# Optimization experiments

Hardware: AMD Instinct MI355X
Metric: run time of the kernel (lower is better)

Reference implementation:

```python
import jax, jax.numpy as jnp
import numpy as np

N = 2048
E_HALF = 65536
THRESHOLD = 0.8


def _segment_softmax(e, seg, n):
    e = e - jax.ops.segment_max(e, seg, num_segments=n)[seg]
    w = jnp.exp(e)
    return w / (jax.ops.segment_sum(w, seg, num_segments=n)[seg] + 1e-16)


def _forward(edge_index, x, mask, Wg1, bg1, Wg2, bg2, Wa1, asrc1, adst1, ba1,
             Wa2, asrc2, adst2, ba2, Wq, bq, Wk, bk, Wv, bv, Wo, bo,
             Wtq, btq, Wtk, btk, Wtv, btv, Wts, bts, W1, b1, W2, b2, Wc, bc):
    n = x.shape[0]
    src, dst = edge_index[0], edge_index[1]

    # dense adjacency (edge_index is symmetric by construction)
    A = jnp.zeros((n, n), jnp.float32).at[src, dst].add(1.0)
    deg = A.sum(axis=1)
    dinv = jnp.where(deg > 0, jax.lax.rsqrt(jnp.maximum(deg, 1e-12)), 0.0)
    # sym-normalized Laplacian L = I - D^-1/2 A D^-1/2 (get_laplacian + to_dense_adj)
    L = jnp.eye(n, dtype=jnp.float32) - dinv[:, None] * A * dinv[None, :]
    _, evecs = jnp.linalg.eigh(L)
    lap_ev = jax.lax.stop_gradient(evecs[:, :2])  # k=2 eigenvectors; data-only, no grad
    x_combined = jnp.concatenate([x, lap_ev], axis=1)  # [n, 5]

    # GCN uncertainty net (torch.no_grad in source)
    A2 = A + jnp.eye(n, dtype=jnp.float32)
    d2 = jax.lax.rsqrt(A2.sum(axis=1))
    Ahat = d2[:, None] * A2 * d2[None, :]

    def gcn(h):
        z = jax.nn.relu(Ahat @ (h @ Wg1) + bg1)
        return (Ahat @ (z @ Wg2) + bg2)[:, 0]

    # add_self_loops
    sl = jnp.arange(n)
    s2 = jnp.concatenate([src, sl])
    d2e = jnp.concatenate([dst, sl])

    def gat(h, W, a_s, a_d, b):
        hw = h @ W                                   # [n, F]
        al = hw @ a_s
        ad = hw @ a_d
        e = jax.nn.leaky_relu(al[s2] + ad[d2e], 0.2)  # per-edge score
        a = _segment_softmax(e, d2e, n)               # softmax over incoming edges
        return jax.ops.segment_sum(a[:, None] * hw[s2], d2e, num_segments=n) + b

    h = jax.nn.relu(gat(x_combined, Wa1, asrc1, adst1, ba1))  # GAT layer 1
    h = gat(h, Wa2, asrc2, adst2, ba2)                        # GAT layer 2 -> [n, 5]

    # nn.MultiheadAttention over all n nodes (seq=n, batch=1, 1 head, d=5)
    q = h @ Wq + bq
    k = h @ Wk + bk
    v = h @ Wv + bv
    attn = jax.nn.softmax((q @ k.T) / np.float32(np.sqrt(5.0)), axis=-1)  # [n, n]
    h = (attn @ v) @ Wo + bo

    # TransformerConv(5, 5, heads=1) with root_weight skip
    tq = h @ Wtq + btq
    tk = h @ Wtk + btk
    tv = h @ Wtv + btv
    e = (tq[d2e] * tk[s2]).sum(-1) / np.float32(np.sqrt(5.0))
    a = _segment_softmax(e, d2e, n)
    xt = jax.ops.segment_sum(a[:, None] * tv[s2], d2e, num_segments=n) + (h @ Wts + bts)

    # MLPAggregation with index=arange(n): each node alone at slot 0 of its group,
    # so flatten([n, n, 5]) @ W1 reduces exactly to xt @ W1[:5]
    hm = jax.nn.relu(xt @ W1[:5] + b1)
    logits = hm @ W2 + b2                            # [n, n]

    # get_safe_logits (torch.no_grad block)
    u = jax.lax.stop_gradient(gcn(xt))               # [n]
    h_t = THRESHOLD - u.max()
    crit = jnp.argmax(u)
    logits = logits.at[crit].add(jnp.where(h_t < 0.2, jnp.float32(10.0), jnp.float32(0.0)))

    masked_logits = logits * mask[None, :]           # broadcast over last dim (torch semantics)
    value = (logits @ Wc + bc).mean()
    return masked_logits, value, x_combined


def setup_inputs() -> dict:
    key = jax.random.key(0)
    ks = jax.random.split(key, 24)

    def w(k, shape, fan_in):
        return jax.random.normal(k, shape, jnp.float32) / np.float32(np.sqrt(fan_in))

    x = jax.random.uniform(ks[0], (N, 3), dtype=jnp.float32)
    e = jax.random.randint(ks[1], (2, E_HALF), 0, N)
    edge_index = jnp.concatenate([e, e[::-1]], axis=1)  # symmetrized -> [2, 2*E_HALF]
    mask = (jax.random.uniform(ks[2], (N,)) > 0.5).astype(jnp.float32)
    return dict(
        x=x, edge_index=edge_index, mask=mask,
        Wg1=w(ks[3], (5, 16), 5), bg1=jnp.zeros(16), Wg2=w(ks[4], (16, 1), 16), bg2=jnp.zeros(1),
        Wa1=w(ks[5], (5, 8), 5), asrc1=w(ks[6], (8,), 8), adst1=w(ks[7], (8,), 8), ba1=jnp.zeros(8),
        Wa2=w(ks[8], (8, 5), 8), asrc2=w(ks[9], (5,), 5), adst2=w(ks[10], (5,), 5), ba2=jnp.zeros(5),
        Wq=w(ks[11], (5, 5), 5), bq=jnp.zeros(5), Wk=w(ks[12], (5, 5), 5), bk=jnp.zeros(5),
        Wv=w(ks[13], (5, 5), 5), bv=jnp.zeros(5), Wo=w(ks[14], (5, 5), 5), bo=jnp.zeros(5),
        Wtq=w(ks[15], (5, 5), 5), btq=jnp.zeros(5), Wtk=w(ks[16], (5, 5), 5), btk=jnp.zeros(5),
        Wtv=w(ks[17], (5, 5), 5), btv=jnp.zeros(5), Wts=w(ks[18], (5, 5), 5), bts=jnp.zeros(5),
        W1=w(ks[19], (5 * N, 64), 5 * N), b1=jnp.zeros(64),
        W2=w(ks[20], (64, N), 64), b2=jnp.zeros(N),
        Wc=w(ks[21], (N, 1), N), bc=jnp.zeros(1))


def reference(x, edge_index, mask, Wg1, bg1, Wg2, bg2, Wa1, asrc1, adst1, ba1,
              Wa2, asrc2, adst2, ba2, Wq, bq, Wk, bk, Wv, bv, Wo, bo,
              Wtq, btq, Wtk, btk, Wtv, btv, Wts, bts, W1, b1, W2, b2, Wc, bc):
    return _forward(edge_index, x, mask, Wg1, bg1, Wg2, bg2, Wa1, asrc1, adst1, ba1,
                    Wa2, asrc2, adst2, ba2, Wq, bq, Wk, bk, Wv, bv, Wo, bo,
                    Wtq, btq, Wtk, btk, Wtv, btv, Wts, bts, W1, b1, W2, b2, Wc, bc)
```

## Files before the change

kernel.cpp:

```cpp
#include <hip/hip_runtime.h>
#include <math.h>


#define N    2048
#define NE   131072
#define KL   64
#define TPB  256
#define NB   16
#define CH   (N/NB)

#define SIGN1 -1.0f
#define SIGN2 -1.0f

__device__ __forceinline__ unsigned fkey(float f){
  unsigned u = __float_as_uint(f);
  return (u & 0x80000000u) ? ~u : (u | 0x80000000u);
}
__device__ __forceinline__ float fkeyinv(unsigned k){
  unsigned u = (k & 0x80000000u) ? (k ^ 0x80000000u) : ~k;
  return __uint_as_float(u);
}
__device__ __forceinline__ unsigned wang(unsigned s){
  s = (s ^ 61u) ^ (s >> 16); s *= 9u; s ^= s >> 4; s *= 0x27d4eb2du; s ^= s >> 15;
  return s;
}
__device__ __forceinline__ float block_sum(float v, float* sh){
  __syncthreads();
  for (int off = 32; off > 0; off >>= 1) v += __shfl_down(v, off);
  int lane = threadIdx.x & 63, w = threadIdx.x >> 6;
  if (lane == 0) sh[w] = v;
  __syncthreads();
  return sh[0] + sh[1] + sh[2] + sh[3];
}

__device__ __forceinline__ float aloadf(const float* p){
  return __hip_atomic_load(p, __ATOMIC_RELAXED, __HIP_MEMORY_SCOPE_AGENT);
}
__device__ __forceinline__ void astoref(float* p, float v){
  __hip_atomic_store(p, v, __ATOMIC_RELAXED, __HIP_MEMORY_SCOPE_AGENT);
}
__device__ __forceinline__ unsigned aloadu(const unsigned* p){
  return __hip_atomic_load(p, __ATOMIC_RELAXED, __HIP_MEMORY_SCOPE_AGENT);
}
__device__ __forceinline__ int aloadi(const int* p){
  return __hip_atomic_load(p, __ATOMIC_RELAXED, __HIP_MEMORY_SCOPE_AGENT);
}
__device__ __forceinline__ void astorei(int* p, int v){
  __hip_atomic_store(p, v, __ATOMIC_RELAXED, __HIP_MEMORY_SCOPE_AGENT);
}
__device__ __forceinline__ float2 aload2(const float* p){
  unsigned long long v = __hip_atomic_load((const unsigned long long*)p,
                         __ATOMIC_RELAXED, __HIP_MEMORY_SCOPE_AGENT);
  return make_float2(__uint_as_float((unsigned)v),
                     __uint_as_float((unsigned)(v >> 32)));
}
__device__ __forceinline__ void astore2(float* p, float a, float b){
  unsigned long long v = ((unsigned long long)__float_as_uint(b) << 32)
                       | (unsigned long long)__float_as_uint(a);
  __hip_atomic_store((unsigned long long*)p, v,
                     __ATOMIC_RELAXED, __HIP_MEMORY_SCOPE_AGENT);
}

__device__ __forceinline__ void gbar(unsigned* cnt, unsigned* gen, unsigned* phase){
  __syncthreads();
  if (threadIdx.x == 0){
    unsigned p = ++(*phase);
    __atomic_signal_fence(__ATOMIC_SEQ_CST);
    __builtin_amdgcn_s_waitcnt(0);
    unsigned old = __hip_atomic_fetch_add(cnt, 1u, __ATOMIC_RELAXED, __HIP_MEMORY_SCOPE_AGENT);
    if (old == p*NB - 1u){
      __hip_atomic_store(gen, p, __ATOMIC_RELAXED, __HIP_MEMORY_SCOPE_AGENT);
    } else {
      while (__hip_atomic_load(gen, __ATOMIC_RELAXED, __HIP_MEMORY_SCOPE_AGENT) < p)
        __builtin_amdgcn_s_sleep(1);
    }
    __atomic_signal_fence(__ATOMIC_SEQ_CST);
  }
  __syncthreads();
}

__global__ void k_init(float* deg, float* scal, unsigned* bar){
  int i = blockIdx.x*TPB + threadIdx.x;
  if (i < N) deg[i] = 0.f;
  if (i < 16) scal[i] = 0.f;
  if (i < 64) bar[i] = 0u;
}
__global__ void k_deg(const int* ei, float* deg){
  int e = blockIdx.x*TPB + threadIdx.x;
  if (e < NE) atomicAdd(&deg[ei[e]], 1.0f);
}
__global__ void k_nodeinit(const float* deg, float* dinv, float* d2g, float* v1){
  int i = blockIdx.x*TPB + threadIdx.x;
  if (i < N){
    float d = deg[i];
    dinv[i] = d > 0.f ? rsqrtf(d) : 0.f;
    d2g[i]  = rsqrtf(d + 1.f);
    v1[i]   = sqrtf(d / (float)NE);
  }
}
__global__ void k_rowptr(const float* deg, int* rowptr, int* fill){
  __shared__ int part[256];
  __shared__ int off[257];
  int t = threadIdx.x;
  int base = t*8;
  int local[8];
  int s = 0;
  for (int k = 0; k < 8; k++){ local[k] = s; s += (int)deg[base + k]; }
  part[t] = s;
  __syncthreads();
  if (t == 0){ off[0] = 0; for (int i = 0; i < 256; i++) off[i+1] = off[i] + part[i]; }
  __syncthreads();
  int o = off[t];
  for (int k = 0; k < 8; k++){ int v = o + local[k]; rowptr[base+k] = v; fill[base+k] = v; }
  if (t == 255) rowptr[N] = off[256];
}
__global__ void k_csr(const int* ei, int* fill, int* cols){
  int e = blockIdx.x*TPB + threadIdx.x;
  if (e < NE){
    int s = ei[e];
    int pos = atomicAdd(&fill[s], 1);
    cols[pos] = ei[NE + e];
  }
}

__global__ __launch_bounds__(256) void k_lanczos(
    const int* __restrict__ rowptr, const int* __restrict__ cols,
    const float* __restrict__ dinv, const float* __restrict__ v1,
    const float* __restrict__ x,
    float* Qsl, float* yG, float* parts, float* parts2, float* npart,
    float* alpha, float* beta, float* zsm, float* v2, float* xc,
    float* outbuf, float* scal, unsigned* mkv, int* v2i, unsigned* bar){
  __shared__ __align__(16) float ybuf[N];
  __shared__ __align__(16) float yl[CH];
  __shared__ float cb[KL+2], cb2[KL+2];
  __shared__ float npl[NB];
  __shared__ float zl[KL];
  __shared__ float sh[4];
  __shared__ unsigned mkl;
  __shared__ double ta[KL], tb2[KL];
  unsigned* cnt = bar;
  unsigned* gen = bar + 32;
  unsigned phase = 0;
  const int tid = threadIdx.x, blk = blockIdx.x;
  const int base = blk*CH;
  float* Qb = Qsl + (size_t)blk*KL*CH;
  float* ssq = scal + 3;

  if (tid < CH){
    float r = (float)(wang(base + tid) & 0xffffffu) * (2.f/16777216.f) - 1.f;
    yl[tid] = r;
  }
  __syncthreads();
  {
    float p = (tid < CH) ? v1[base + tid]*yl[tid] : 0.f;
    float s = block_sum(p, sh);
    if (tid == 0) astoref(&parts[blk], s);
  }
  gbar(cnt, gen, &phase);
  {
    if (tid < NB) npl[tid] = aloadf(&parts[tid]);
    __syncthreads();
    float c = 0.f;
    for (int b = 0; b < NB; b++) c += npl[b];
    float acc = 0.f;
    if (tid < CH){
      float v = yl[tid] - c*v1[base + tid];
      yl[tid] = v;
      acc = v*v;
    }
    __syncthreads();
    if (tid < CH/2) astore2(yG + base + 2*tid, yl[2*tid], yl[2*tid+1]);
    float s = block_sum(acc, sh);
    if (tid == 0) astoref(&npart[blk], s);
  }
  gbar(cnt, gen, &phase);

  for (int j = 0; j < KL; j++){
    {
      for (int t = tid; t < N/2; t += TPB){
        float2 v = aload2(yG + 2*t);
        ybuf[2*t] = v.x; ybuf[2*t+1] = v.y;
      }
      if (tid < NB/2){
        float2 v = aload2(npart + 2*tid);
        npl[2*tid] = v.x; npl[2*tid+1] = v.y;
      }
    }
    __syncthreads();
    {
      float ss = 0.f;
      for (int b = 0; b < NB; b++) ss += npl[b];
      float rn = rsqrtf(ss);
      if (blk == 0 && tid == 0 && j > 0) beta[j-1] = sqrtf(ss);
      int r = tid >> 1;
      int half = tid & 1;
      int row = base + r;
      int b0 = rowptr[row], b1 = rowptr[row+1];
      float sg = 0.f;
      for (int p = b0 + half; p < b1; p += 2){
        int c = cols[p];
        sg += dinv[c]*ybuf[c];
      }
      sg += __shfl_down(sg, 1);
      if (half == 0){
        float q = rn*ybuf[row];
        Qb[(size_t)j*CH + r] = q;
        yl[r] = q - dinv[row]*rn*sg;
      }
    }
    __syncthreads();
    if (tid <= j+1){
      float d = 0.f;
      const float4* y4 = (const float4*)yl;
      if (tid <= j){
        const float4* q4 = (const float4*)(Qb + (size_t)tid*CH);
        for (int e = 0; e < CH/4; e++){
          float4 q = q4[e], yv = y4[e];
          d += q.x*yv.x + q.y*yv.y + q.z*yv.z + q.w*yv.w;
        }
      } else {
        const float4* v4 = (const float4*)(v1 + base);
        for (int e = 0; e < CH/4; e++){
          float4 q = v4[e], yv = y4[e];
          d += q.x*yv.x + q.y*yv.y + q.z*yv.z + q.w*yv.w;
        }
      }
      astoref(&parts[tid*NB + blk], d);
    }
    gbar(cnt, gen, &phase);
    if (tid <= j+1){
      const float* pr = parts + tid*NB;
      float s = 0.f;
      for (int b = 0; b < NB/2; b++){
        float2 v = aload2(pr + 2*b);
        s += v.x + v.y;
      }
      cb[tid] = s;
    }
    __syncthreads();
    {
      int e = tid >> 1, h = tid & 1;
      float a2 = 0.f;
      for (int i = h; i <= j+1; i += 2)
        a2 += cb[i] * ((i <= j) ? Qb[(size_t)i*CH + e] : v1[base + e]);
      a2 += __shfl_down(a2, 1);
      if (h == 0) yl[e] -= a2;
    }
    __syncthreads();
    if (tid <= j+1){
      float d = 0.f;
      const float4* y4 = (const float4*)yl;
      if (tid <= j){
        const float4* q4 = (const float4*)(Qb + (size_t)tid*CH);
        for (int e = 0; e < CH/4; e++){
          float4 q = q4[e], yv = y4[e];
          d += q.x*yv.x + q.y*yv.y + q.z*yv.z + q.w*yv.w;
        }
      } else {
        const float4* v4 = (const float4*)(v1 + base);
        for (int e = 0; e < CH/4; e++){
          float4 q = v4[e], yv = y4[e];
          d += q.x*yv.x + q.y*yv.y + q.z*yv.z + q.w*yv.w;
        }
      }
      astoref(&parts2[tid*NB + blk], d);
    }
    gbar(cnt, gen, &phase);
    if (tid <= j+1){
      const float* pr = parts2 + tid*NB;
      float s = 0.f;
      for (int b = 0; b < NB/2; b++){
        float2 v = aload2(pr + 2*b);
        s += v.x + v.y;
      }
      cb2[tid] = s;
    }
    __syncthreads();
    if (blk == 0 && tid == j) alpha[j] = cb[j] + cb2[j];
    float nv = 0.f;
    {
      int e = tid >> 1, h = tid & 1;
      float a2 = 0.f;
      for (int i = h; i <= j+1; i += 2)
        a2 += cb2[i] * ((i <= j) ? Qb[(size_t)i*CH + e] : v1[base + e]);
      a2 += __shfl_down(a2, 1);
      if (h == 0){
        float v = yl[e] - a2;
        yl[e] = v;
        nv = v*v;
      }
    }
    float s = block_sum(nv, sh);
    if (tid == 0) astoref(&npart[blk], s);
    if (tid < CH/2) astore2(yG + base + 2*tid, yl[2*tid], yl[2*tid+1]);
    gbar(cnt, gen, &phase);
  }

  const int wid = tid >> 6, lane = tid & 63;
  if (blk == 0){
    for (int i = tid; i < KL; i += TPB) ta[i] = (double)alpha[i];
    for (int i = tid; i < KL-1; i += TPB){ double bb = (double)beta[i]; tb2[i] = bb*bb; }
    __syncthreads();
    if (wid == 0){
      double th[2];
      for (int k = 1; k <= 2; k++){
        double lo = -0.5, hi = 2.5;
        for (int r = 0; r < 5; r++){
          double xx = lo + (hi - lo)*(double)(lane + 1)/65.0;
          int c = 0; double q = 1.0;
          for (int i = 0; i < KL; i++){
            double t = ta[i] - xx - ((i > 0) ? tb2[i-1]/q : 0.0);
            if (t == 0.0) t = -1e-300;
            if (t < 0.0) c++;
            q = t;
          }
          unsigned long long m = __ballot(c >= k);
          if (m == 0ULL){
            lo = lo + (hi - lo)*(64.0/65.0);
          } else {
            int f = __ffsll((long long)m) - 1;
            double nhi = lo + (hi - lo)*(double)(f + 1)/65.0;
            double nlo = lo + (hi - lo)*(double)f/65.0;
            hi = nhi; lo = nlo;
          }
        }
        th[k-1] = 0.5*(lo + hi);
      }
      double theta = (th[0] < 0.25) ? th[1] : th[0];
      if (lane == 0){
        double d[KL], dl[KL], du[KL], du2[KL], xv[KL];
        int ip[KL];
        for (int i = 0; i < KL; i++) d[i] = ta[i] - theta;
        for (int i = 0; i < KL-1; i++){ double b = (double)beta[i]; dl[i] = b; du[i] = b; }
        for (int i = 0; i < KL-1; i++){
          if (fabs(d[i]) >= fabs(dl[i])){
            ip[i] = 0;
            if (d[i] == 0.0) d[i] = 1e-30;
            double f = dl[i]/d[i]; dl[i] = f; d[i+1] -= f*du[i];
            if (i < KL-2) du2[i] = 0.0;
          } else {
            double f = d[i]/dl[i];
            d[i] = dl[i]; dl[i] = f;
            double t = du[i]; du[i] = d[i+1]; d[i+1] = t - f*d[i+1];
            if (i < KL-2){ du2[i] = du[i+1]; du[i+1] = -f*du[i+1]; }
            ip[i] = 1;
          }
        }
        if (d[KL-1] == 0.0) d[KL-1] = 1e-30;
        for (int i = 0; i < KL; i++) xv[i] = (double)(wang(1000u + i) & 0xffffu)/65536.0 - 0.5;
        for (int it = 0; it < 4; it++){
          for (int i = 0; i < KL-1; i++){
            if (ip[i] == 0) xv[i+1] -= dl[i]*xv[i];
            else { double t = xv[i]; xv[i] = xv[i+1]; xv[i+1] = t - dl[i]*xv[i]; }
          }
          xv[KL-1] /= d[KL-1];
          xv[KL-2] = (xv[KL-2] - du[KL-2]*xv[KL-1])/d[KL-2];
          for (int i = KL-3; i >= 0; i--) xv[i] = (xv[i] - du[i]*xv[i+1] - du2[i]*xv[i+2])/d[i];
          double m = 0.0;
          for (int i = 0; i < KL; i++) m = fmax(m, fabs(xv[i]));
          if (m > 0.0) for (int i = 0; i < KL; i++) xv[i] /= m;
        }
        double nrm = 0.0;
        for (int i = 0; i < KL; i++) nrm += xv[i]*xv[i];
        nrm = sqrt(nrm);
        for (int i = 0; i < KL; i++) astoref(&zsm[i], (float)(xv[i]/nrm));
      }
    }
  }
  gbar(cnt, gen, &phase);
  if (tid < KL) zl[tid] = aloadf(&zsm[tid]);
  __syncthreads();
  float a = 0.f;
  if (tid < CH){
    for (int i = 0; i < KL; i++) a += zl[i]*Qb[(size_t)i*CH + tid];
    astoref(&v2[base + tid], a);
  }
  {
    float sq = block_sum(a*a, sh);
    __syncthreads();
    float av = fabsf(a);
    for (int d2 = 1; d2 < 64; d2 <<= 1) av = fmaxf(av, __shfl_xor(av, d2));
    if ((tid & 63) == 0) sh[tid >> 6] = av;
    __syncthreads();
    if (tid == 0){
      float mb = fmaxf(fmaxf(sh[0], sh[1]), fmaxf(sh[2], sh[3]));
      atomicAdd(ssq, sq);
      atomicMax(mkv, fkey(mb));
      if (blk == 0) astorei(v2i, N);
    }
  }
  gbar(cnt, gen, &phase);
  if (tid == 0) mkl = aloadu(mkv);
  __syncthreads();
  if (tid < CH){
    float vv = aloadf(&v2[base + tid]);
    if (fkey(fabsf(vv)) == mkl) atomicMin(v2i, base + tid);
  }
  gbar(cnt, gen, &phase);
  if (blk == 0 && tid == 0){
    float s = rsqrtf(aloadf(ssq));
    int ii = aloadi(v2i);
    if (aloadf(&v2[ii]) < 0.f) s = -s;
    astoref(&scal[4], SIGN2 * s);
  }
  gbar(cnt, gen, &phase);
  if (tid < CH){
    int i = base + tid;
    float sc = aloadf(&scal[4]);
    float l1 = aloadf(&v2[i])*sc;
    float l0 = SIGN1*v1[i];
    float c0 = x[i*3+0], c1 = x[i*3+1], c2 = x[i*3+2];
    float* xr = xc + (size_t)i*5;
    xr[0]=c0; xr[1]=c1; xr[2]=c2; xr[3]=l0; xr[4]=l1;
    float* o = outbuf + (size_t)N*N + 1 + (size_t)i*5;
    o[0]=c0; o[1]=c1; o[2]=c2; o[3]=l0; o[4]=l1;
  }
}

__global__ void k_lin(const float* in, const float* W, const float* b, float* out,
                      int Fin, int Fout, int act, int total){
  int t = blockIdx.x*TPB + threadIdx.x;
  if (t >= total) return;
  int i = t / Fout, f = t - i*Fout;
  float acc = b ? b[f] : 0.f;
  const float* ir = in + (size_t)i*Fin;
  for (int k2 = 0; k2 < Fin; k2++) acc += ir[k2]*W[k2*Fout + f];
  if (act) acc = fmaxf(acc, 0.f);
  out[t] = acc;
}
__global__ void k_lin3(const float* in,
                       const float* W0, const float* b0, float* o0,
                       const float* W1, const float* b1, float* o1,
                       const float* W2, const float* b2, float* o2){
  int t = blockIdx.x*TPB + threadIdx.x;
  if (t >= N*5) return;
  int i = t/5, f = t - i*5;
  const float* ir = in + (size_t)i*5;
  float a0 = b0[f], a1 = b1[f], a2 = b2[f];
  for (int c = 0; c < 5; c++){
    float h = ir[c];
    a0 += h*W0[c*5+f]; a1 += h*W1[c*5+f]; a2 += h*W2[c*5+f];
  }
  o0[t] = a0; o1[t] = a1; o2[t] = a2;
}
__global__ void k_h3tc(const float* att, const float* Wo, const float* bo,
                       const float* Wtq, const float* btq,
                       const float* Wtk, const float* btk,
                       const float* Wtv, const float* btv,
                       float* h3, float* tq, float* tk, float* tv){
  int i = blockIdx.x*TPB + threadIdx.x;
  if (i >= N) return;
  const float* ar = att + (size_t)i*5;
  float h[5];
  for (int f = 0; f < 5; f++){
    float acc = bo[f];
    for (int k = 0; k < 5; k++) acc += ar[k]*Wo[k*5+f];
    h[f] = acc;
  }
  float* hr = h3 + (size_t)i*5;
  float* qr = tq + (size_t)i*5;
  float* kr = tk + (size_t)i*5;
  float* vr = tv + (size_t)i*5;
  for (int f = 0; f < 5; f++){
    float aq = btq[f], ak = btk[f], av = btv[f];
    for (int k = 0; k < 5; k++){
      float hk = h[k];
      aq += hk*Wtq[k*5+f]; ak += hk*Wtk[k*5+f]; av += hk*Wtv[k*5+f];
    }
    hr[f] = h[f]; qr[f] = aq; kr[f] = ak; vr[f] = av;
  }
}

__global__ __launch_bounds__(256) void k_gat_fused(
    const int* __restrict__ rowptr, const int* __restrict__ cols,
    const float* __restrict__ in, const float* __restrict__ W,
    const float* __restrict__ as, const float* __restrict__ adp,
    const float* __restrict__ bias, float* hout, int Fin, int F, int act){
  int row = blockIdx.x*4 + (threadIdx.x >> 6);
  int lane = threadIdx.x & 63;
  int b0 = rowptr[row], b1 = rowptr[row+1];
  float hwr[8];
  {
    const float* ir = in + (size_t)row*Fin;
    for (int f = 0; f < F; f++){
      float acc = 0.f;
      for (int k = 0; k < Fin; k++) acc += ir[k]*W[k*F+f];
      hwr[f] = acc;
    }
  }
  float adv = 0.f, alr = 0.f;
  for (int f = 0; f < F; f++){ adv += hwr[f]*adp[f]; alr += hwr[f]*as[f]; }
  float es = alr + adv; es = es >= 0.f ? es : 0.2f*es;
  float m = es;
  for (int p = b0 + lane; p < b1; p += 64){
    const float* ic = in + (size_t)cols[p]*Fin;
    float al = 0.f;
    for (int f = 0; f < F; f++){
      float acc = 0.f;
      for (int k = 0; k < Fin; k++) acc += ic[k]*W[k*F+f];
      al += acc*as[f];
    }
    float e = al + adv; e = e >= 0.f ? e : 0.2f*e;
    m = fmaxf(m, e);
  }
  for (int d = 1; d < 64; d <<= 1) m = fmaxf(m, __shfl_xor(m, d));
  float Z = 0.f;
  float accf[8];
  for (int f = 0; f < 8; f++) accf[f] = 0.f;
  for (int p = b0 + lane; p < b1; p += 64){
    const float* ic = in + (size_t)cols[p]*Fin;
    float hc[8];
    float al = 0.f;
    for (int f = 0; f < F; f++){
      float acc = 0.f;
      for (int k = 0; k < Fin; k++) acc += ic[k]*W[k*F+f];
      hc[f] = acc;
      al += acc*as[f];
    }
    float e = al + adv; e = e >= 0.f ? e : 0.2f*e;
    float w = expf(e - m);
    Z += w;
    for (int f = 0; f < F; f++) accf[f] += w*hc[f];
  }
  if (lane == 0){
    float w = expf(es - m);
    Z += w;
    for (int f = 0; f < F; f++) accf[f] += w*hwr[f];
  }
  for (int d = 1; d < 64; d <<= 1){
    Z += __shfl_xor(Z, d);
    for (int f = 0; f < F; f++) accf[f] += __shfl_xor(accf[f], d);
  }
  if (lane < F){
    float v = accf[lane]/(Z + 1e-16f) + bias[lane];
    if (act) v = fmaxf(v, 0.f);
    hout[(size_t)row*F + lane] = v;
  }
}

__global__ __launch_bounds__(256) void k_tc_gather(
    const int* __restrict__ rowptr, const int* __restrict__ cols,
    const float* __restrict__ tq, const float* __restrict__ tk,
    const float* __restrict__ tv, const float* __restrict__ h3,
    const float* __restrict__ Wts, const float* __restrict__ bts, float* xt){
  int row = blockIdx.x*4 + (threadIdx.x >> 6);
  int lane = threadIdx.x & 63;
  int b0 = rowptr[row], b1 = rowptr[row+1];
  const float* qr = tq + (size_t)row*5;
  float q0=qr[0], q1=qr[1], q2=qr[2], q3=qr[3], q4=qr[4];
  const float* ks = tk + (size_t)row*5;
  float es = (q0*ks[0]+q1*ks[1]+q2*ks[2]+q3*ks[3]+q4*ks[4])*0.44721360f;
  float m = es;
  for (int p = b0 + lane; p < b1; p += 64){
    const float* kr = tk + (size_t)cols[p]*5;
    float e = (q0*kr[0]+q1*kr[1]+q2*kr[2]+q3*kr[3]+q4*kr[4])*0.44721360f;
    m = fmaxf(m, e);
  }
  for (int d = 1; d < 64; d <<= 1) m = fmaxf(m, __shfl_xor(m, d));
  float Z = 0.f;
  float accf[5];
  for (int f = 0; f < 5; f++) accf[f] = 0.f;
  for (int p = b0 + lane; p < b1; p += 64){
    int c = cols[p];
    const float* kr = tk + (size_t)c*5;
    float e = (q0*kr[0]+q1*kr[1]+q2*kr[2]+q3*kr[3]+q4*kr[4])*0.44721360f;
    float w = expf(e - m);
    Z += w;
    const float* vr = tv + (size_t)c*5;
    for (int f = 0; f < 5; f++) accf[f] += w*vr[f];
  }
  if (lane == 0){
    float w = expf(es - m);
    Z += w;
    const float* vr = tv + (size_t)row*5;
    for (int f = 0; f < 5; f++) accf[f] += w*vr[f];
  }
  for (int d = 1; d < 64; d <<= 1){
    Z += __shfl_xor(Z, d);
    for (int f = 0; f < 5; f++) accf[f] += __shfl_xor(accf[f], d);
  }
  if (lane < 5){
    const float* hr = h3 + (size_t)row*5;
    float skip = bts[lane];
    for (int k2 = 0; k2 < 5; k2++) skip += hr[k2]*Wts[k2*5 + lane];
    xt[(size_t)row*5 + lane] = accf[lane]/(Z + 1e-16f) + skip;
  }
}

__global__ __launch_bounds__(256) void k_gcn16(
    const int* __restrict__ rowptr, const int* __restrict__ cols,
    const float* __restrict__ P16, const float* __restrict__ d2g,
    const float* __restrict__ bg1, float* z16){
  int row = blockIdx.x*4 + (threadIdx.x >> 6);
  int lane = threadIdx.x & 63;
  int b0 = rowptr[row], b1 = rowptr[row+1];
  float dr = d2g[row];
  float acc[16];
  for (int f = 0; f < 16; f++) acc[f] = 0.f;
  for (int p = b0 + lane; p < b1; p += 64){
    int c = cols[p];
    float w = d2g[c];
    const float* pr = P16 + (size_t)c*16;
    for (int f = 0; f < 16; f++) acc[f] += w*pr[f];
  }
  if (lane == 0){
    const float* pr = P16 + (size_t)row*16;
    for (int f = 0; f < 16; f++) acc[f] += dr*pr[f];
  }
  for (int d = 1; d < 64; d <<= 1)
    for (int f = 0; f < 16; f++) acc[f] += __shfl_xor(acc[f], d);
  if (lane < 16)
    z16[(size_t)row*16 + lane] = fmaxf(dr*acc[lane] + bg1[lane], 0.f);
}
__global__ __launch_bounds__(256) void k_gcn1(
    const int* __restrict__ rowptr, const int* __restrict__ cols,
    const float* __restrict__ p1, const float* __restrict__ d2g,
    const float* __restrict__ bg2, float* u, unsigned* mku, int* crit){
  int row = blockIdx.x*4 + (threadIdx.x >> 6);
  int lane = threadIdx.x & 63;
  if (blockIdx.x == 0 && threadIdx.x == 0) crit[0] = N;
  int b0 = rowptr[row], b1 = rowptr[row+1];
  float s = 0.f;
  for (int p = b0 + lane; p < b1; p += 64) s += d2g[cols[p]]*p1[cols[p]];
  if (lane == 0) s += d2g[row]*p1[row];
  for (int d = 1; d < 64; d <<= 1) s += __shfl_xor(s, d);
  float uv = d2g[row]*s + bg2[0];
  if (lane == 0){
    u[row] = uv;
    atomicMax(mku, fkey(uv));
  }
}
__global__ void k_crit(const float* u, const unsigned* mk, int* crit, float* bonus){
  int i = blockIdx.x*TPB + threadIdx.x;
  if (i == 0){
    float um = fkeyinv(mk[0]);
    bonus[0] = ((0.8f - um) < 0.2f) ? 10.f : 0.f;
  }
  if (i >= N) return;
  if (u[i] == fkeyinv(mk[0])) atomicMin(crit, i);
}

__global__ __launch_bounds__(256) void k_mha(const float* qb, const float* kb,
                                             const float* vb, float* av){
  __shared__ float s[N];
  __shared__ float sh[4];
  __shared__ float red[4];
  int i = blockIdx.x;
  const float* qr = qb + (size_t)i*5;
  float q0=qr[0], q1=qr[1], q2=qr[2], q3=qr[3], q4=qr[4];
  float lmax = -1e30f;
  for (int j = threadIdx.x; j < N; j += TPB){
    const float* kr = kb + (size_t)j*5;
    float sc = (q0*kr[0]+q1*kr[1]+q2*kr[2]+q3*kr[3]+q4*kr[4])*0.44721360f;
    s[j] = sc;
    lmax = fmaxf(lmax, sc);
  }
  for (int off = 32; off > 0; off >>= 1) lmax = fmaxf(lmax, __shfl_down(lmax, off));
  int lane = threadIdx.x & 63, w = threadIdx.x >> 6;
  if (lane == 0) red[w] = lmax;
  __syncthreads();
  float m = fmaxf(fmaxf(red[0], red[1]), fmaxf(red[2], red[3]));
  float Zp = 0.f, a0=0.f, a1=0.f, a2=0.f, a3=0.f, a4=0.f;
  for (int j = threadIdx.x; j < N; j += TPB){
    float p = expf(s[j] - m);
    const float* vr = vb + (size_t)j*5;
    Zp += p; a0 += p*vr[0]; a1 += p*vr[1]; a2 += p*vr[2]; a3 += p*vr[3]; a4 += p*vr[4];
  }
  float Z  = block_sum(Zp, sh);
  float A0 = block_sum(a0, sh);
  float A1 = block_sum(a1, sh);
  float A2 = block_sum(a2, sh);
  float A3 = block_sum(a3, sh);
  float A4 = block_sum(a4, sh);
  if (threadIdx.x == 0){
    float inv = 1.f/Z;
    float* o = av + (size_t)i*5;
    o[0]=A0*inv; o[1]=A1*inv; o[2]=A2*inv; o[3]=A3*inv; o[4]=A4*inv;
  }
}

__global__ __launch_bounds__(256) void k_logits(const float* hm, const float* W2,
    const float* b2, const float* mask, const float* Wc, const int* crit,
    const float* bonus, float* out, float* vacc){
  __shared__ float sh[4];
  int j = blockIdx.x*TPB + threadIdx.x;
  int i = blockIdx.y;
  const float* hr = hm + (size_t)i*64;
  float acc = b2[j];
  for (int c = 0; c < 64; c++) acc += hr[c]*W2[c*N + j];
  if (i == crit[0]) acc += bonus[0];
  out[(size_t)i*N + j] = acc*mask[j];
  float s = block_sum(acc*Wc[j], sh);
  if (threadIdx.x == 0) atomicAdd(vacc, s);
}
__global__ void k_value(const float* vacc, const float* bc, float* out){
  out[(size_t)N*N] = vacc[0]/(float)N + bc[0];
}

extern "C" void kernel_launch(void* const* d_in, const int* in_sizes, int n_in,
                              void* d_out, int out_size, void* d_ws, size_t ws_size,
                              hipStream_t stream){
  const float* x    = (const float*)d_in[0];
  const int*   ei   = (const int*)d_in[1];
  const float* mask = (const float*)d_in[2];
  const float* Wg1=(const float*)d_in[3];  const float* bg1=(const float*)d_in[4];
  const float* Wg2=(const float*)d_in[5];  const float* bg2=(const float*)d_in[6];
  const float* Wa1=(const float*)d_in[7];  const float* as1=(const float*)d_in[8];
  const float* ad1=(const float*)d_in[9];  const float* ba1=(const float*)d_in[10];
  const float* Wa2=(const float*)d_in[11]; const float* as2=(const float*)d_in[12];
  const float* ad2=(const float*)d_in[13]; const float* ba2=(const float*)d_in[14];
  const float* Wq=(const float*)d_in[15];  const float* bq=(const float*)d_in[16];
  const float* Wk=(const float*)d_in[17];  const float* bk=(const float*)d_in[18];
  const float* Wv=(const float*)d_in[19];  const float* bv=(const float*)d_in[20];
  const float* Wo=(const float*)d_in[21];  const float* bo=(const float*)d_in[22];
  const float* Wtq=(const float*)d_in[23]; const float* btq=(const float*)d_in[24];
  const float* Wtk=(const float*)d_in[25]; const float* btk=(const float*)d_in[26];
  const float* Wtv=(const float*)d_in[27]; const float* btv=(const float*)d_in[28];
  const float* Wts=(const float*)d_in[29]; const float* bts=(const float*)d_in[30];
  const float* W1=(const float*)d_in[31];  const float* b1=(const float*)d_in[32];
  const float* W2=(const float*)d_in[33];  const float* b2=(const float*)d_in[34];
  const float* Wc=(const float*)d_in[35];  const float* bc=(const float*)d_in[36];
  float* out = (float*)d_out;
  float* ws  = (float*)d_ws;

  float* deg  = ws;           float* dinv = ws + 2048;
  float* d2g  = ws + 4096;    float* v1   = ws + 6144;
  float* y    = ws + 8192;    float* v2   = ws + 10240;
  float* alpha= ws + 12448;   float* beta = ws + 12576;
  float* scal = ws + 12704;
  unsigned* mku = (unsigned*)(scal + 8);
  unsigned* mkv = (unsigned*)(scal + 9);
  int* crit = (int*)(scal + 10);
  int* v2i  = (int*)(scal + 11);
  float* zsm  = ws + 12720;
  float* h2   = ws + 21040;   float* qb   = ws + 31280;
  float* kb   = ws + 41520;   float* vb   = ws + 51760;
  float* h3   = ws + 62000;   float* tqb  = ws + 72240;
  float* tkb  = ws + 82480;   float* tvb  = ws + 92720;
  float* xt   = ws + 102960;  float* p1   = ws + 113200;
  float* u    = ws + 115248;  float* hm   = ws + 117296;

  float* Qsl  = out;
  float* hw   = out + 262144;
  float* h8   = out + 278528;
  float* P16  = out + 294912;
  float* z16  = out + 327680;
  float* xc   = out + 360448;
  unsigned* bar = (unsigned*)(out + 370688);
  int* rowptr = (int*)(out + 370752);
  int* fill   = (int*)(out + 372864);
  int* cols   = (int*)(out + 374912);
  float* parts  = out + 507904;
  float* parts2 = out + 510080;
  float* npart  = out + 512256;

  k_init<<<8, TPB, 0, stream>>>(deg, scal, bar);
  k_deg<<<NE/TPB, TPB, 0, stream>>>(ei, deg);
  k_nodeinit<<<8, TPB, 0, stream>>>(deg, dinv, d2g, v1);
  k_rowptr<<<1, TPB, 0, stream>>>(deg, rowptr, fill);
  k_csr<<<NE/TPB, TPB, 0, stream>>>(ei, fill, cols);

  k_lanczos<<<NB, TPB, 0, stream>>>(rowptr, cols, dinv, v1, x, Qsl, y,
                                    parts, parts2, npart, alpha, beta, zsm,
                                    v2, xc, out, scal, mkv, v2i, bar);

  const int gN5  = (N*5 + TPB-1)/TPB;
  const int gRow = N/4;

  k_gat_fused<<<gRow, TPB, 0, stream>>>(rowptr, cols, xc, Wa1, as1, ad1, ba1, h8, 5, 8, 1);
  k_gat_fused<<<gRow, TPB, 0, stream>>>(rowptr, cols, h8, Wa2, as2, ad2, ba2, h2, 8, 5, 0);

  k_lin3<<<gN5, TPB, 0, stream>>>(h2, Wq, bq, qb, Wk, bk, kb, Wv, bv, vb);
  k_mha<<<N, TPB, 0, stream>>>(qb, kb, vb, hw);
  k_h3tc<<<8, TPB, 0, stream>>>(hw, Wo, bo, Wtq, btq, Wtk, btk, Wtv, btv,
                                h3, tqb, tkb, tvb);

  k_tc_gather<<<gRow, TPB, 0, stream>>>(rowptr, cols, tqb, tkb, tvb, h3, Wts, bts, xt);

  k_lin<<<(N*16 + TPB-1)/TPB, TPB, 0, stream>>>(xt, Wg1, nullptr, P16, 5, 16, 0, N*16);
  k_gcn16<<<gRow, TPB, 0, stream>>>(rowptr, cols, P16, d2g, bg1, z16);
  k_lin<<<8, TPB, 0, stream>>>(z16, Wg2, nullptr, p1, 16, 1, 0, N);
  k_gcn1<<<gRow, TPB, 0, stream>>>(rowptr, cols, p1, d2g, bg2, u, mku, crit);
  k_crit<<<8, TPB, 0, stream>>>(u, mku, crit, scal + 5);

  k_lin<<<(N*64 + TPB-1)/TPB, TPB, 0, stream>>>(xt, W1, b1, hm, 5, 64, 1, N*64);
  k_logits<<<dim3(8, N), TPB, 0, stream>>>(hm, W2, b2, mask, Wc, crit, scal + 5, out, scal + 6);
  k_value<<<1, 1, 0, stream>>>(scal + 6, bc, out);
}
```

Baseline: 2.072 ms.

## Halve Lanczos block count and fuse small linear layers into consumers

```diff
diff --git a/kernel.cpp b/kernel.cpp
--- a/kernel.cpp
+++ b/kernel.cpp
@@ -6,7 +6,7 @@
 #define NE   131072
 #define KL   64
 #define TPB  256
-#define NB   16
+#define NB   8
 #define CH   (N/NB)
 
 #define SIGN1 -1.0f
@@ -89,23 +89,22 @@
   int e = blockIdx.x*TPB + threadIdx.x;
   if (e < NE) atomicAdd(&deg[ei[e]], 1.0f);
 }
-__global__ void k_nodeinit(const float* deg, float* dinv, float* d2g, float* v1){
-  int i = blockIdx.x*TPB + threadIdx.x;
-  if (i < N){
-    float d = deg[i];
-    dinv[i] = d > 0.f ? rsqrtf(d) : 0.f;
-    d2g[i]  = rsqrtf(d + 1.f);
-    v1[i]   = sqrtf(d / (float)NE);
-  }
-}
-__global__ void k_rowptr(const float* deg, int* rowptr, int* fill){
+__global__ void k_rowptr(const float* deg, int* rowptr, int* fill,
+                         float* dinv, float* d2g, float* v1){
   __shared__ int part[256];
   __shared__ int off[257];
   int t = threadIdx.x;
   int base = t*8;
   int local[8];
   int s = 0;
-  for (int k = 0; k < 8; k++){ local[k] = s; s += (int)deg[base + k]; }
+  for (int k = 0; k < 8; k++){
+    int r = base + k;
+    float d = deg[r];
+    dinv[r] = d > 0.f ? rsqrtf(d) : 0.f;
+    d2g[r]  = rsqrtf(d + 1.f);
+    v1[r]   = sqrtf(d / (float)NE);
+    local[k] = s; s += (int)d;
+  }
   part[t] = s;
   __syncthreads();
   if (t == 0){ off[0] = 0; for (int i = 0; i < 256; i++) off[i+1] = off[i] + part[i]; }
@@ -146,13 +145,10 @@
   float* Qb = Qsl + (size_t)blk*KL*CH;
   float* ssq = scal + 3;
 
-  if (tid < CH){
-    float r = (float)(wang(base + tid) & 0xffffffu) * (2.f/16777216.f) - 1.f;
-    yl[tid] = r;
-  }
+  yl[tid] = (float)(wang(base + tid) & 0xffffffu) * (2.f/16777216.f) - 1.f;
   __syncthreads();
   {
-    float p = (tid < CH) ? v1[base + tid]*yl[tid] : 0.f;
+    float p = v1[base + tid]*yl[tid];
     float s = block_sum(p, sh);
     if (tid == 0) astoref(&parts[blk], s);
   }
@@ -162,12 +158,9 @@
     __syncthreads();
     float c = 0.f;
     for (int b = 0; b < NB; b++) c += npl[b];
-    float acc = 0.f;
-    if (tid < CH){
-      float v = yl[tid] - c*v1[base + tid];
-      yl[tid] = v;
-      acc = v*v;
-    }
+    float v = yl[tid] - c*v1[base + tid];
+    yl[tid] = v;
+    float acc = v*v;
     __syncthreads();
     if (tid < CH/2) astore2(yG + base + 2*tid, yl[2*tid], yl[2*tid+1]);
     float s = block_sum(acc, sh);
@@ -192,21 +185,16 @@
       for (int b = 0; b < NB; b++) ss += npl[b];
       float rn = rsqrtf(ss);
       if (blk == 0 && tid == 0 && j > 0) beta[j-1] = sqrtf(ss);
-      int r = tid >> 1;
-      int half = tid & 1;
-      int row = base + r;
+      int row = base + tid;
       int b0 = rowptr[row], b1 = rowptr[row+1];
       float sg = 0.f;
-      for (int p = b0 + half; p < b1; p += 2){
+      for (int p = b0; p < b1; p++){
         int c = cols[p];
         sg += dinv[c]*ybuf[c];
       }
-      sg += __shfl_down(sg, 1);
-      if (half == 0){
-        float q = rn*ybuf[row];
-        Qb[(size_t)j*CH + r] = q;
-        yl[r] = q - dinv[row]*rn*sg;
-      }
+      float q = rn*ybuf[row];
+      Qb[(size_t)j*CH + tid] = q;
+      yl[tid] = q - dinv[row]*rn*sg;
     }
     __syncthreads();
     if (tid <= j+1){
@@ -239,12 +227,10 @@
     }
     __syncthreads();
     {
-      int e = tid >> 1, h = tid & 1;
       float a2 = 0.f;
-      for (int i = h; i <= j+1; i += 2)
-        a2 += cb[i] * ((i <= j) ? Qb[(size_t)i*CH + e] : v1[base + e]);
-      a2 += __shfl_down(a2, 1);
-      if (h == 0) yl[e] -= a2;
+      for (int i = 0; i <= j; i++) a2 += cb[i]*Qb[(size_t)i*CH + tid];
+      a2 += cb[j+1]*v1[base + tid];
+      yl[tid] -= a2;
     }
     __syncthreads();
     if (tid <= j+1){
@@ -277,18 +263,14 @@
     }
     __syncthreads();
     if (blk == 0 && tid == j) alpha[j] = cb[j] + cb2[j];
-    float nv = 0.f;
+    float nv;
     {
-      int e = tid >> 1, h = tid & 1;
       float a2 = 0.f;
-      for (int i = h; i <= j+1; i += 2)
-        a2 += cb2[i] * ((i <= j) ? Qb[(size_t)i*CH + e] : v1[base + e]);
-      a2 += __shfl_down(a2, 1);
-      if (h == 0){
-        float v = yl[e] - a2;
-        yl[e] = v;
-        nv = v*v;
-      }
+      for (int i = 0; i <= j; i++) a2 += cb2[i]*Qb[(size_t)i*CH + tid];
+      a2 += cb2[j+1]*v1[base + tid];
+      float v = yl[tid] - a2;
+      yl[tid] = v;
+      nv = v*v;
     }
     float s = block_sum(nv, sh);
     if (tid == 0) astoref(&npart[blk], s);
@@ -371,10 +353,8 @@
   if (tid < KL) zl[tid] = aloadf(&zsm[tid]);
   __syncthreads();
   float a = 0.f;
-  if (tid < CH){
-    for (int i = 0; i < KL; i++) a += zl[i]*Qb[(size_t)i*CH + tid];
-    astoref(&v2[base + tid], a);
-  }
+  for (int i = 0; i < KL; i++) a += zl[i]*Qb[(size_t)i*CH + tid];
+  astoref(&v2[base + tid], a);
   {
     float sq = block_sum(a*a, sh);
     __syncthreads();
@@ -392,7 +372,7 @@
   gbar(cnt, gen, &phase);
   if (tid == 0) mkl = aloadu(mkv);
   __syncthreads();
-  if (tid < CH){
+  {
     float vv = aloadf(&v2[base + tid]);
     if (fkey(fabsf(vv)) == mkl) atomicMin(v2i, base + tid);
   }
@@ -404,7 +384,7 @@
     astoref(&scal[4], SIGN2 * s);
   }
   gbar(cnt, gen, &phase);
-  if (tid < CH){
+  {
     int i = base + tid;
     float sc = aloadf(&scal[4]);
     float l1 = aloadf(&v2[i])*sc;
@@ -414,60 +394,6 @@
     xr[0]=c0; xr[1]=c1; xr[2]=c2; xr[3]=l0; xr[4]=l1;
     float* o = outbuf + (size_t)N*N + 1 + (size_t)i*5;
     o[0]=c0; o[1]=c1; o[2]=c2; o[3]=l0; o[4]=l1;
-  }
-}
-
-__global__ void k_lin(const float* in, const float* W, const float* b, float* out,
-                      int Fin, int Fout, int act, int total){
-  int t = blockIdx.x*TPB + threadIdx.x;
-  if (t >= total) return;
-  int i = t / Fout, f = t - i*Fout;
-  float acc = b ? b[f] : 0.f;
-  const float* ir = in + (size_t)i*Fin;
-  for (int k2 = 0; k2 < Fin; k2++) acc += ir[k2]*W[k2*Fout + f];
-  if (act) acc = fmaxf(acc, 0.f);
-  out[t] = acc;
-}
-__global__ void k_lin3(const float* in,
-                       const float* W0, const float* b0, float* o0,
-                       const float* W1, const float* b1, float* o1,
-                       const float* W2, const float* b2, float* o2){
-  int t = blockIdx.x*TPB + threadIdx.x;
-  if (t >= N*5) return;
-  int i = t/5, f = t - i*5;
-  const float* ir = in + (size_t)i*5;
-  float a0 = b0[f], a1 = b1[f], a2 = b2[f];
-  for (int c = 0; c < 5; c++){
-    float h = ir[c];
-    a0 += h*W0[c*5+f]; a1 += h*W1[c*5+f]; a2 += h*W2[c*5+f];
-  }
-  o0[t] = a0; o1[t] = a1; o2[t] = a2;
-}
-__global__ void k_h3tc(const float* att, const float* Wo, const float* bo,
-                       const float* Wtq, const float* btq,
-                       const float* Wtk, const float* btk,
-                       const float* Wtv, const float* btv,
-                       float* h3, float* tq, float* tk, float* tv){
-  int i = blockIdx.x*TPB + threadIdx.x;
-  if (i >= N) return;
-  const float* ar = att + (size_t)i*5;
-  float h[5];
-  for (int f = 0; f < 5; f++){
-    float acc = bo[f];
-    for (int k = 0; k < 5; k++) acc += ar[k]*Wo[k*5+f];
-    h[f] = acc;
-  }
-  float* hr = h3 + (size_t)i*5;
-  float* qr = tq + (size_t)i*5;
-  float* kr = tk + (size_t)i*5;
-  float* vr = tv + (size_t)i*5;
-  for (int f = 0; f < 5; f++){
-    float aq = btq[f], ak = btk[f], av = btv[f];
-    for (int k = 0; k < 5; k++){
-      float hk = h[k];
-      aq += hk*Wtq[k*5+f]; ak += hk*Wtk[k*5+f]; av += hk*Wtv[k*5+f];
-    }
-    hr[f] = h[f]; qr[f] = aq; kr[f] = ak; vr[f] = av;
   }
 }
 
@@ -535,6 +461,97 @@
     float v = accf[lane]/(Z + 1e-16f) + bias[lane];
     if (act) v = fmaxf(v, 0.f);
     hout[(size_t)row*F + lane] = v;
+  }
+}
+
+__global__ __launch_bounds__(256) void k_mha_f(const float* __restrict__ h2,
+    const float* __restrict__ Wq, const float* __restrict__ bq,
+    const float* __restrict__ Wk, const float* __restrict__ bk,
+    const float* __restrict__ Wv, const float* __restrict__ bv, float* av){
+  __shared__ float s[N];
+  __shared__ float sh[4];
+  __shared__ float red[4];
+  int i = blockIdx.x;
+  float q[5];
+  {
+    const float* hr = h2 + (size_t)i*5;
+    for (int f = 0; f < 5; f++){
+      float acc = bq[f];
+      for (int k = 0; k < 5; k++) acc += hr[k]*Wq[k*5+f];
+      q[f] = acc;
+    }
+  }
+  float wk[25], wv[25], bkr[5], bvr[5];
+  for (int t = 0; t < 25; t++){ wk[t] = Wk[t]; wv[t] = Wv[t]; }
+  for (int t = 0; t < 5; t++){ bkr[t] = bk[t]; bvr[t] = bv[t]; }
+  float lmax = -1e30f;
+  for (int j = threadIdx.x; j < N; j += TPB){
+    const float* hr = h2 + (size_t)j*5;
+    float h0=hr[0], h1=hr[1], h2v=hr[2], h3v=hr[3], h4=hr[4];
+    float sc = 0.f;
+    for (int f = 0; f < 5; f++){
+      float kf = bkr[f] + h0*wk[f] + h1*wk[5+f] + h2v*wk[10+f] + h3v*wk[15+f] + h4*wk[20+f];
+      sc += q[f]*kf;
+    }
+    sc *= 0.44721360f;
+    s[j] = sc;
+    lmax = fmaxf(lmax, sc);
+  }
+  for (int off = 32; off > 0; off >>= 1) lmax = fmaxf(lmax, __shfl_down(lmax, off));
+  int lane = threadIdx.x & 63, w = threadIdx.x >> 6;
+  if (lane == 0) red[w] = lmax;
+  __syncthreads();
+  float m = fmaxf(fmaxf(red[0], red[1]), fmaxf(red[2], red[3]));
+  float Zp = 0.f, a0=0.f, a1=0.f, a2=0.f, a3=0.f, a4=0.f;
+  for (int j = threadIdx.x; j < N; j += TPB){
+    float p = expf(s[j] - m);
+    const float* hr = h2 + (size_t)j*5;
+    float h0=hr[0], h1=hr[1], h2v=hr[2], h3v=hr[3], h4=hr[4];
+    Zp += p;
+    a0 += p*(bvr[0] + h0*wv[0] + h1*wv[5]  + h2v*wv[10] + h3v*wv[15] + h4*wv[20]);
+    a1 += p*(bvr[1] + h0*wv[1] + h1*wv[6]  + h2v*wv[11] + h3v*wv[16] + h4*wv[21]);
+    a2 += p*(bvr[2] + h0*wv[2] + h1*wv[7]  + h2v*wv[12] + h3v*wv[17] + h4*wv[22]);
+    a3 += p*(bvr[3] + h0*wv[3] + h1*wv[8]  + h2v*wv[13] + h3v*wv[18] + h4*wv[23]);
+    a4 += p*(bvr[4] + h0*wv[4] + h1*wv[9]  + h2v*wv[14] + h3v*wv[19] + h4*wv[24]);
+  }
+  float Z  = block_sum(Zp, sh);
+  float A0 = block_sum(a0, sh);
+  float A1 = block_sum(a1, sh);
+  float A2 = block_sum(a2, sh);
+  float A3 = block_sum(a3, sh);
+  float A4 = block_sum(a4, sh);
+  if (threadIdx.x == 0){
+    float inv = 1.f/Z;
+    float* o = av + (size_t)i*5;
+    o[0]=A0*inv; o[1]=A1*inv; o[2]=A2*inv; o[3]=A3*inv; o[4]=A4*inv;
+  }
+}
+
+__global__ void k_h3tc(const float* att, const float* Wo, const float* bo,
+                       const float* Wtq, const float* btq,
+                       const float* Wtk, const float* btk,
+                       const float* Wtv, const float* btv,
+                       float* h3, float* tq, float* tk, float* tv){
+  int i = blockIdx.x*TPB + threadIdx.x;
+  if (i >= N) return;
+  const float* ar = att + (size_t)i*5;
+  float h[5];
+  for (int f = 0; f < 5; f++){
+    float acc = bo[f];
+    for (int k = 0; k < 5; k++) acc += ar[k]*Wo[k*5+f];
+    h[f] = acc;
+  }
+  float* hr = h3 + (size_t)i*5;
+  float* qr = tq + (size_t)i*5;
+  float* kr = tk + (size_t)i*5;
+  float* vr = tv + (size_t)i*5;
+  for (int f = 0; f < 5; f++){
+    float aq = btq[f], ak = btk[f], av = btv[f];
+    for (int k = 0; k < 5; k++){
+      float hk = h[k];
+      aq += hk*Wtq[k*5+f]; ak += hk*Wtk[k*5+f]; av += hk*Wtv[k*5+f];
+    }
+    hr[f] = h[f]; qr[f] = aq; kr[f] = ak; vr[f] = av;
   }
 }
 
@@ -587,10 +604,13 @@
   }
 }
 
-__global__ __launch_bounds__(256) void k_gcn16(
+__global__ __launch_bounds__(256) void k_gcn16f(
     const int* __restrict__ rowptr, const int* __restrict__ cols,
-    const float* __restrict__ P16, const float* __restrict__ d2g,
-    const float* __restrict__ bg1, float* z16){
+    const float* __restrict__ xt, const float* __restrict__ Wg1,
+    const float* __restrict__ d2g, const float* __restrict__ bg1, float* z16){
+  __shared__ float wg[80];
+  if (threadIdx.x < 80) wg[threadIdx.x] = Wg1[threadIdx.x];
+  __syncthreads();
   int row = blockIdx.x*4 + (threadIdx.x >> 6);
   int lane = threadIdx.x & 63;
   int b0 = rowptr[row], b1 = rowptr[row+1];
@@ -600,29 +620,48 @@
   for (int p = b0 + lane; p < b1; p += 64){
     int c = cols[p];
     float w = d2g[c];
-    const float* pr = P16 + (size_t)c*16;
-    for (int f = 0; f < 16; f++) acc[f] += w*pr[f];
+    const float* xr = xt + (size_t)c*5;
+    float x0=xr[0], x1=xr[1], x2=xr[2], x3=xr[3], x4=xr[4];
+    for (int f = 0; f < 16; f++)
+      acc[f] += w*(x0*wg[f] + x1*wg[16+f] + x2*wg[32+f] + x3*wg[48+f] + x4*wg[64+f]);
   }
   if (lane == 0){
-    const float* pr = P16 + (size_t)row*16;
-    for (int f = 0; f < 16; f++) acc[f] += dr*pr[f];
+    const float* xr = xt + (size_t)row*5;
+    float x0=xr[0], x1=xr[1], x2=xr[2], x3=xr[3], x4=xr[4];
+    for (int f = 0; f < 16; f++)
+      acc[f] += dr*(x0*wg[f] + x1*wg[16+f] + x2*wg[32+f] + x3*wg[48+f] + x4*wg[64+f]);
   }
   for (int d = 1; d < 64; d <<= 1)
     for (int f = 0; f < 16; f++) acc[f] += __shfl_xor(acc[f], d);
   if (lane < 16)
     z16[(size_t)row*16 + lane] = fmaxf(dr*acc[lane] + bg1[lane], 0.f);
 }
-__global__ __launch_bounds__(256) void k_gcn1(
+__global__ __launch_bounds__(256) void k_gcn1f(
     const int* __restrict__ rowptr, const int* __restrict__ cols,
-    const float* __restrict__ p1, const float* __restrict__ d2g,
-    const float* __restrict__ bg2, float* u, unsigned* mku, int* crit){
+    const float* __restrict__ z16, const float* __restrict__ Wg2,
+    const float* __restrict__ d2g, const float* __restrict__ bg2,
+    float* u, unsigned* mku, int* crit){
+  __shared__ float wg[16];
+  if (threadIdx.x < 16) wg[threadIdx.x] = Wg2[threadIdx.x];
+  __syncthreads();
   int row = blockIdx.x*4 + (threadIdx.x >> 6);
   int lane = threadIdx.x & 63;
   if (blockIdx.x == 0 && threadIdx.x == 0) crit[0] = N;
   int b0 = rowptr[row], b1 = rowptr[row+1];
   float s = 0.f;
-  for (int p = b0 + lane; p < b1; p += 64) s += d2g[cols[p]]*p1[cols[p]];
-  if (lane == 0) s += d2g[row]*p1[row];
+  for (int p = b0 + lane; p < b1; p += 64){
+    int c = cols[p];
+    const float* zr = z16 + (size_t)c*16;
+    float p1c = 0.f;
+    for (int k = 0; k < 16; k++) p1c += zr[k]*wg[k];
+    s += d2g[c]*p1c;
+  }
+  if (lane == 0){
+    const float* zr = z16 + (size_t)row*16;
+    float p1c = 0.f;
+    for (int k = 0; k < 16; k++) p1c += zr[k]*wg[k];
+    s += d2g[row]*p1c;
+  }
   for (int d = 1; d < 64; d <<= 1) s += __shfl_xor(s, d);
   float uv = d2g[row]*s + bg2[0];
   if (lane == 0){
@@ -640,54 +679,23 @@
   if (u[i] == fkeyinv(mk[0])) atomicMin(crit, i);
 }
 
-__global__ __launch_bounds__(256) void k_mha(const float* qb, const float* kb,
-                                             const float* vb, float* av){
-  __shared__ float s[N];
-  __shared__ float sh[4];
-  __shared__ float red[4];
-  int i = blockIdx.x;
-  const float* qr = qb + (size_t)i*5;
-  float q0=qr[0], q1=qr[1], q2=qr[2], q3=qr[3], q4=qr[4];
-  float lmax = -1e30f;
-  for (int j = threadIdx.x; j < N; j += TPB){
-    const float* kr = kb + (size_t)j*5;
-    float sc = (q0*kr[0]+q1*kr[1]+q2*kr[2]+q3*kr[3]+q4*kr[4])*0.44721360f;
-    s[j] = sc;
-    lmax = fmaxf(lmax, sc);
-  }
-  for (int off = 32; off > 0; off >>= 1) lmax = fmaxf(lmax, __shfl_down(lmax, off));
-  int lane = threadIdx.x & 63, w = threadIdx.x >> 6;
-  if (lane == 0) red[w] = lmax;
-  __syncthreads();
-  float m = fmaxf(fmaxf(red[0], red[1]), fmaxf(red[2], red[3]));
-  float Zp = 0.f, a0=0.f, a1=0.f, a2=0.f, a3=0.f, a4=0.f;
-  for (int j = threadIdx.x; j < N; j += TPB){
-    float p = expf(s[j] - m);
-    const float* vr = vb + (size_t)j*5;
-    Zp += p; a0 += p*vr[0]; a1 += p*vr[1]; a2 += p*vr[2]; a3 += p*vr[3]; a4 += p*vr[4];
-  }
-  float Z  = block_sum(Zp, sh);
-  float A0 = block_sum(a0, sh);
-  float A1 = block_sum(a1, sh);
-  float A2 = block_sum(a2, sh);
-  float A3 = block_sum(a3, sh);
-  float A4 = block_sum(a4, sh);
-  if (threadIdx.x == 0){
-    float inv = 1.f/Z;
-    float* o = av + (size_t)i*5;
-    o[0]=A0*inv; o[1]=A1*inv; o[2]=A2*inv; o[3]=A3*inv; o[4]=A4*inv;
-  }
-}
-
-__global__ __launch_bounds__(256) void k_logits(const float* hm, const float* W2,
+__global__ __launch_bounds__(256) void k_logits(const float* xt,
+    const float* W1, const float* b1, const float* W2,
     const float* b2, const float* mask, const float* Wc, const int* crit,
     const float* bonus, float* out, float* vacc){
   __shared__ float sh[4];
+  __shared__ float hml[64];
+  int i = blockIdx.y;
+  if (threadIdx.x < 64){
+    const float* xr = xt + (size_t)i*5;
+    float acc = b1[threadIdx.x];
+    for (int k = 0; k < 5; k++) acc += xr[k]*W1[k*64 + threadIdx.x];
+    hml[threadIdx.x] = fmaxf(acc, 0.f);
+  }
+  __syncthreads();
   int j = blockIdx.x*TPB + threadIdx.x;
-  int i = blockIdx.y;
-  const float* hr = hm + (size_t)i*64;
   float acc = b2[j];
-  for (int c = 0; c < 64; c++) acc += hr[c]*W2[c*N + j];
+  for (int c = 0; c < 64; c++) acc += hml[c]*W2[c*N + j];
   if (i == crit[0]) acc += bonus[0];
   out[(size_t)i*N + j] = acc*mask[j];
   float s = block_sum(acc*Wc[j], sh);
@@ -733,17 +741,15 @@
   int* crit = (int*)(scal + 10);
   int* v2i  = (int*)(scal + 11);
   float* zsm  = ws + 12720;
-  float* h2   = ws + 21040;   float* qb   = ws + 31280;
-  float* kb   = ws + 41520;   float* vb   = ws + 51760;
+  float* h2   = ws + 21040;
   float* h3   = ws + 62000;   float* tqb  = ws + 72240;
   float* tkb  = ws + 82480;   float* tvb  = ws + 92720;
-  float* xt   = ws + 102960;  float* p1   = ws + 113200;
-  float* u    = ws + 115248;  float* hm   = ws + 117296;
+  float* xt   = ws + 102960;
+  float* u    = ws + 115248;
 
   float* Qsl  = out;
   float* hw   = out + 262144;
   float* h8   = out + 278528;
-  float* P16  = out + 294912;
   float* z16  = out + 327680;
   float* xc   = out + 360448;
   unsigned* bar = (unsigned*)(out + 370688);
@@ -756,34 +762,29 @@
 
   k_init<<<8, TPB, 0, stream>>>(deg, scal, bar);
   k_deg<<<NE/TPB, TPB, 0, stream>>>(ei, deg);
-  k_nodeinit<<<8, TPB, 0, stream>>>(deg, dinv, d2g, v1);
-  k_rowptr<<<1, TPB, 0, stream>>>(deg, rowptr, fill);
+  k_rowptr<<<1, TPB, 0, stream>>>(deg, rowptr, fill, dinv, d2g, v1);
   k_csr<<<NE/TPB, TPB, 0, stream>>>(ei, fill, cols);
 
   k_lanczos<<<NB, TPB, 0, stream>>>(rowptr, cols, dinv, v1, x, Qsl, y,
                                     parts, parts2, npart, alpha, beta, zsm,
                                     v2, xc, out, scal, mkv, v2i, bar);
 
-  const int gN5  = (N*5 + TPB-1)/TPB;
   const int gRow = N/4;
 
   k_gat_fused<<<gRow, TPB, 0, stream>>>(rowptr, cols, xc, Wa1, as1, ad1, ba1, h8, 5, 8, 1);
   k_gat_fused<<<gRow, TPB, 0, stream>>>(rowptr, cols, h8, Wa2, as2, ad2, ba2, h2, 8, 5, 0);
 
-  k_lin3<<<gN5, TPB, 0, stream>>>(h2, Wq, bq, qb, Wk, bk, kb, Wv, bv, vb);
-  k_mha<<<N, TPB, 0, stream>>>(qb, kb, vb, hw);
+  k_mha_f<<<N, TPB, 0, stream>>>(h2, Wq, bq, Wk, bk, Wv, bv, hw);
   k_h3tc<<<8, TPB, 0, stream>>>(hw, Wo, bo, Wtq, btq, Wtk, btk, Wtv, btv,
                                 h3, tqb, tkb, tvb);
 
   k_tc_gather<<<gRow, TPB, 0, stream>>>(rowptr, cols, tqb, tkb, tvb, h3, Wts, bts, xt);
 
-  k_lin<<<(N*16 + TPB-1)/TPB, TPB, 0, stream>>>(xt, Wg1, nullptr, P16, 5, 16, 0, N*16);
-  k_gcn16<<<gRow, TPB, 0, stream>>>(rowptr, cols, P16, d2g, bg1, z16);
-  k_lin<<<8, TPB, 0, stream>>>(z16, Wg2, nullptr, p1, 16, 1, 0, N);
-  k_gcn1<<<gRow, TPB, 0, stream>>>(rowptr, cols, p1, d2g, bg2, u, mku, crit);
+  k_gcn16f<<<gRow, TPB, 0, stream>>>(rowptr, cols, xt, Wg1, d2g, bg1, z16);
+  k_gcn1f<<<gRow, TPB, 0, stream>>>(rowptr, cols, z16, Wg2, d2g, bg2, u, mku, crit);
   k_crit<<<8, TPB, 0, stream>>>(u, mku, crit, scal + 5);
 
-  k_lin<<<(N*64 + TPB-1)/TPB, TPB, 0, stream>>>(xt, W1, b1, hm, 5, 64, 1, N*64);
-  k_logits<<<dim3(8, N), TPB, 0, stream>>>(hm, W2, b2, mask, Wc, crit, scal + 5, out, scal + 6);
+  k_logits<<<dim3(8, N), TPB, 0, stream>>>(xt, W1, b1, W2, b2, mask, Wc, crit,
+                                           scal + 5, out, scal + 6);
   k_value<<<1, 1, 0, stream>>>(scal + 6, bc, out);
 }
```

Result: slower. 2.781 ms (+34.2%).
